# Kernel tuning notes

Hardware: AMD Instinct MI355X
Metric: run time of the kernel (lower is better)

Reference implementation:

```python
import jax, jax.numpy as jnp
import numpy as np

N, T, U, C, V = 8, 256, 64, 512, 1024

def setup_inputs() -> dict:
    key = jax.random.key(0)
    k1, k2, k3, k4 = jax.random.split(key, 4)
    encoder_out = jax.random.normal(k1, (N, T, C), dtype=jnp.float32)
    pred_out = jax.random.normal(k2, (N, U, C), dtype=jnp.float32)
    # nn.Linear(C, V): weight (V, C), bias (V,)
    bound = 1.0 / np.sqrt(C)
    W = jax.random.uniform(k3, (V, C), minval=-bound, maxval=bound, dtype=jnp.float32)
    b = jax.random.uniform(k4, (V,), minval=-bound, maxval=bound, dtype=jnp.float32)
    return {"encoder_out": encoder_out, "pred_out": pred_out, "W": W, "b": b}

def reference(encoder_out, pred_out, W, b):
    # broadcast add: (N,T,1,C) + (N,1,U,C) -> (N,T,U,C)
    x = jnp.tanh(encoder_out[:, :, None, :] + pred_out[:, None, :, :])
    # Linear projection to vocab: (N,T,U,C) @ (C,V) + b
    logits = jnp.einsum("ntuc,vc->ntuv", x, W) + b
    return logits
```

## Files before the change

### kernel.cpp

```cpp
#include <hip/hip_runtime.h>

#define C_DIM 512
#define V_DIM 1024

typedef __attribute__((ext_vector_type(8))) short short8;
typedef __attribute__((ext_vector_type(4))) float f32x4;

__device__ __forceinline__ short f2bf(float f) {
  unsigned int u = __float_as_uint(f);
  u += 0x7fffu + ((u >> 16) & 1u);
  return (short)(u >> 16);
}

__device__ __forceinline__ float fast_tanh_f(float x) {
  float e = __expf(2.0f * x);
  return fmaf(-2.0f, __builtin_amdgcn_rcpf(e + 1.0f), 1.0f);
}

__global__ __launch_bounds__(256) void wswz_kernel(const float* __restrict__ W,
                                                   char* __restrict__ wsw) {
  const int i = blockIdx.x * 256 + threadIdx.x;
  const int v = i >> 6;
  const int c0 = (i & 63) << 3;
  const float* wp = W + (size_t)v * C_DIM + c0;
  const f32x4 w0 = *(const f32x4*)(wp);
  const f32x4 w1 = *(const f32x4*)(wp + 4);
  short8 pk;
  pk[0] = f2bf(w0[0]); pk[1] = f2bf(w0[1]); pk[2] = f2bf(w0[2]); pk[3] = f2bf(w0[3]);
  pk[4] = f2bf(w1[0]); pk[5] = f2bf(w1[1]); pk[6] = f2bf(w1[2]); pk[7] = f2bf(w1[3]);
  const int vt = v >> 8, vloc = v & 255;
  const int kc = c0 >> 5, q = (c0 >> 3) & 3;
  char* dst = wsw + (size_t)(vt * 16 + kc) * 16384 + vloc * 64 + q * 16;
  *(short8*)dst = pk;
}

__global__ __launch_bounds__(256, 3) void joiner_kernel(
    const float* __restrict__ enc, const float* __restrict__ pred,
    const char* __restrict__ wsw, const float* __restrict__ bias,
    float* __restrict__ out) {
  __shared__ char abuf[2][4096];
  const int tid = threadIdx.x;
  const int lane = tid & 63;
  const int wn = tid >> 6;
  const int l15 = lane & 15, qd = lane >> 4;

  const int bid = blockIdx.x;
  const int wk = ((bid & 7) << 10) | (bid >> 3);
  const int rp = wk >> 2;
  const int vt = wk & 3;
  const int n = rp >> 8;

  const float* pe = enc + (size_t)rp * C_DIM + (tid & 3) * 8;
  const float* pp = pred + ((size_t)(n << 6) + (tid >> 2)) * C_DIM + (tid & 3) * 8;
  char* adst = &abuf[0][0] + tid * 16;

  const char* wbase = wsw + (size_t)vt * (16 * 16384) + (size_t)(wn * 64 + l15) * 64 + qd * 16;

  const char* afr = &abuf[0][0] + l15 * 64 + qd * 16;

  f32x4 acc[4][4];
#pragma unroll
  for (int mt = 0; mt < 4; ++mt)
#pragma unroll
    for (int nt = 0; nt < 4; ++nt) acc[mt][nt] = (f32x4){0.f, 0.f, 0.f, 0.f};

  short8 bfr[2][4];

  {
    const f32x4 e0 = *(const f32x4*)(pe);
    const f32x4 e1 = *(const f32x4*)(pe + 4);
    const f32x4 p0 = *(const f32x4*)(pp);
    const f32x4 p1 = *(const f32x4*)(pp + 4);
    short8 pk;
    pk[0] = f2bf(fast_tanh_f(e0[0] + p0[0]));
    pk[1] = f2bf(fast_tanh_f(e0[1] + p0[1]));
    pk[2] = f2bf(fast_tanh_f(e0[2] + p0[2]));
    pk[3] = f2bf(fast_tanh_f(e0[3] + p0[3]));
    pk[4] = f2bf(fast_tanh_f(e1[0] + p1[0]));
    pk[5] = f2bf(fast_tanh_f(e1[1] + p1[1]));
    pk[6] = f2bf(fast_tanh_f(e1[2] + p1[2]));
    pk[7] = f2bf(fast_tanh_f(e1[3] + p1[3]));
    *(short8*)(adst) = pk;
  }
#pragma unroll
  for (int nt = 0; nt < 4; ++nt)
    bfr[0][nt] = *(const short8*)(wbase + nt * 1024);
  __syncthreads();

#pragma unroll 2
  for (int kc = 0; kc < 16; ++kc) {
    const int cb = kc & 1, nb = cb ^ 1;

    f32x4 e0, e1, p0, p1;
    if (kc < 15) {
      const float* pe1 = pe + (kc + 1) * 32;
      const float* pp1 = pp + (kc + 1) * 32;
      e0 = *(const f32x4*)(pe1);
      e1 = *(const f32x4*)(pe1 + 4);
      p0 = *(const f32x4*)(pp1);
      p1 = *(const f32x4*)(pp1 + 4);
#pragma unroll
      for (int nt = 0; nt < 4; ++nt)
        bfr[nb][nt] = *(const short8*)(wbase + (kc + 1) * 16384 + nt * 1024);
    }

    const char* ab = afr + cb * 4096;
    const short8 a0 = *(const short8*)(ab);
    const short8 a1 = *(const short8*)(ab + 1024);
    const short8 a2 = *(const short8*)(ab + 2048);
    const short8 a3 = *(const short8*)(ab + 3072);

    acc[0][0] = __builtin_amdgcn_mfma_f32_16x16x32_bf16(a0, bfr[cb][0], acc[0][0], 0, 0, 0);
    acc[0][1] = __builtin_amdgcn_mfma_f32_16x16x32_bf16(a0, bfr[cb][1], acc[0][1], 0, 0, 0);
    acc[0][2] = __builtin_amdgcn_mfma_f32_16x16x32_bf16(a0, bfr[cb][2], acc[0][2], 0, 0, 0);
    acc[0][3] = __builtin_amdgcn_mfma_f32_16x16x32_bf16(a0, bfr[cb][3], acc[0][3], 0, 0, 0);
    acc[1][0] = __builtin_amdgcn_mfma_f32_16x16x32_bf16(a1, bfr[cb][0], acc[1][0], 0, 0, 0);
    acc[1][1] = __builtin_amdgcn_mfma_f32_16x16x32_bf16(a1, bfr[cb][1], acc[1][1], 0, 0, 0);
    acc[1][2] = __builtin_amdgcn_mfma_f32_16x16x32_bf16(a1, bfr[cb][2], acc[1][2], 0, 0, 0);
    acc[1][3] = __builtin_amdgcn_mfma_f32_16x16x32_bf16(a1, bfr[cb][3], acc[1][3], 0, 0, 0);
    acc[2][0] = __builtin_amdgcn_mfma_f32_16x16x32_bf16(a2, bfr[cb][0], acc[2][0], 0, 0, 0);
    acc[2][1] = __builtin_amdgcn_mfma_f32_16x16x32_bf16(a2, bfr[cb][1], acc[2][1], 0, 0, 0);
    acc[2][2] = __builtin_amdgcn_mfma_f32_16x16x32_bf16(a2, bfr[cb][2], acc[2][2], 0, 0, 0);
    acc[2][3] = __builtin_amdgcn_mfma_f32_16x16x32_bf16(a2, bfr[cb][3], acc[2][3], 0, 0, 0);
    acc[3][0] = __builtin_amdgcn_mfma_f32_16x16x32_bf16(a3, bfr[cb][0], acc[3][0], 0, 0, 0);
    acc[3][1] = __builtin_amdgcn_mfma_f32_16x16x32_bf16(a3, bfr[cb][1], acc[3][1], 0, 0, 0);
    acc[3][2] = __builtin_amdgcn_mfma_f32_16x16x32_bf16(a3, bfr[cb][2], acc[3][2], 0, 0, 0);
    acc[3][3] = __builtin_amdgcn_mfma_f32_16x16x32_bf16(a3, bfr[cb][3], acc[3][3], 0, 0, 0);

    if (kc < 15) {
      short8 pk;
      pk[0] = f2bf(fast_tanh_f(e0[0] + p0[0]));
      pk[1] = f2bf(fast_tanh_f(e0[1] + p0[1]));
      pk[2] = f2bf(fast_tanh_f(e0[2] + p0[2]));
      pk[3] = f2bf(fast_tanh_f(e0[3] + p0[3]));
      pk[4] = f2bf(fast_tanh_f(e1[0] + p1[0]));
      pk[5] = f2bf(fast_tanh_f(e1[1] + p1[1]));
      pk[6] = f2bf(fast_tanh_f(e1[2] + p1[2]));
      pk[7] = f2bf(fast_tanh_f(e1[3] + p1[3]));
      *(short8*)(adst + nb * 4096) = pk;
    }
    __syncthreads();
  }

  const int colb = (vt << 8) + (wn << 6) + l15;
  const size_t r0 = ((size_t)rp << 6) + (qd << 2);
#pragma unroll
  for (int nt = 0; nt < 4; ++nt) {
    const float bb = bias[colb + nt * 16];
#pragma unroll
    for (int mt = 0; mt < 4; ++mt) {
      float* op = out + (r0 + mt * 16) * V_DIM + colb + nt * 16;
      op[0 * V_DIM] = acc[mt][nt][0] + bb;
      op[1 * V_DIM] = acc[mt][nt][1] + bb;
      op[2 * V_DIM] = acc[mt][nt][2] + bb;
      op[3 * V_DIM] = acc[mt][nt][3] + bb;
    }
  }
}

extern "C" void kernel_launch(void* const* d_in, const int* in_sizes, int n_in,
                              void* d_out, int out_size, void* d_ws, size_t ws_size,
                              hipStream_t stream) {
  const float* enc  = (const float*)d_in[0];
  const float* pred = (const float*)d_in[1];
  const float* W    = (const float*)d_in[2];
  const float* bias = (const float*)d_in[3];
  float* out = (float*)d_out;
  char* wsw = (char*)d_ws;

  wswz_kernel<<<dim3(256), dim3(256), 0, stream>>>(W, wsw);
  joiner_kernel<<<dim3(8192), dim3(256), 0, stream>>>(enc, pred, wsw, bias, out);
}
```

Baseline: 699.6 us.

## Stage full tanh A-tile in LDS once and loop over all vocab tiles

Each block now computes the full 64x512 tanh activation for one (n,t) row into 64KB of dynamic LDS once, then loops over all four vocab tiles, instead of recomputing the activation per vocab tile across four separate blocks. The MFMA switches from 16x16x32 to 32x32x16 bf16, and the weight swizzle is changed to match the new fragment layout. It also adds s_setprio around the MFMA bursts and uses nontemporal output stores. The costs are lower occupancy (2 blocks per CU, large LDS) and a serial activation prologue that no longer overlaps with the MFMA work.

```diff
diff --git a/kernel.cpp b/kernel.cpp
--- a/kernel.cpp
+++ b/kernel.cpp
@@ -5,6 +5,7 @@
 
 typedef __attribute__((ext_vector_type(8))) short short8;
 typedef __attribute__((ext_vector_type(4))) float f32x4;
+typedef __attribute__((ext_vector_type(16))) float f32x16;
 
 __device__ __forceinline__ short f2bf(float f) {
   unsigned int u = __float_as_uint(f);
@@ -29,105 +30,41 @@
   pk[0] = f2bf(w0[0]); pk[1] = f2bf(w0[1]); pk[2] = f2bf(w0[2]); pk[3] = f2bf(w0[3]);
   pk[4] = f2bf(w1[0]); pk[5] = f2bf(w1[1]); pk[6] = f2bf(w1[2]); pk[7] = f2bf(w1[3]);
   const int vt = v >> 8, vloc = v & 255;
-  const int kc = c0 >> 5, q = (c0 >> 3) & 3;
-  char* dst = wsw + (size_t)(vt * 16 + kc) * 16384 + vloc * 64 + q * 16;
+  const int wn = vloc >> 6, nt = (vloc >> 5) & 1, c32 = vloc & 31;
+  const int kc = c0 >> 5, s = (c0 >> 4) & 1, hi = (c0 >> 3) & 1;
+  char* dst = wsw + (size_t)(vt * 16 + kc) * 16384 +
+              wn * 4096 + nt * 2048 + s * 1024 + hi * 512 + c32 * 16;
   *(short8*)dst = pk;
 }
 
-__global__ __launch_bounds__(256, 3) void joiner_kernel(
+__global__ __launch_bounds__(256, 2) void joiner_kernel(
     const float* __restrict__ enc, const float* __restrict__ pred,
     const char* __restrict__ wsw, const float* __restrict__ bias,
     float* __restrict__ out) {
-  __shared__ char abuf[2][4096];
+  extern __shared__ char smem[];
   const int tid = threadIdx.x;
   const int lane = tid & 63;
   const int wn = tid >> 6;
-  const int l15 = lane & 15, qd = lane >> 4;
+  const int l31 = lane & 31, hf = lane >> 5;
 
   const int bid = blockIdx.x;
-  const int wk = ((bid & 7) << 10) | (bid >> 3);
-  const int rp = wk >> 2;
-  const int vt = wk & 3;
+  const int rp = ((bid & 7) << 8) | (bid >> 3);
   const int n = rp >> 8;
 
-  const float* pe = enc + (size_t)rp * C_DIM + (tid & 3) * 8;
-  const float* pp = pred + ((size_t)(n << 6) + (tid >> 2)) * C_DIM + (tid & 3) * 8;
-  char* adst = &abuf[0][0] + tid * 16;
-
-  const char* wbase = wsw + (size_t)vt * (16 * 16384) + (size_t)(wn * 64 + l15) * 64 + qd * 16;
-
-  const char* afr = &abuf[0][0] + l15 * 64 + qd * 16;
-
-  f32x4 acc[4][4];
-#pragma unroll
-  for (int mt = 0; mt < 4; ++mt)
-#pragma unroll
-    for (int nt = 0; nt < 4; ++nt) acc[mt][nt] = (f32x4){0.f, 0.f, 0.f, 0.f};
-
-  short8 bfr[2][4];
-
   {
-    const f32x4 e0 = *(const f32x4*)(pe);
-    const f32x4 e1 = *(const f32x4*)(pe + 4);
-    const f32x4 p0 = *(const f32x4*)(pp);
-    const f32x4 p1 = *(const f32x4*)(pp + 4);
-    short8 pk;
-    pk[0] = f2bf(fast_tanh_f(e0[0] + p0[0]));
-    pk[1] = f2bf(fast_tanh_f(e0[1] + p0[1]));
-    pk[2] = f2bf(fast_tanh_f(e0[2] + p0[2]));
-    pk[3] = f2bf(fast_tanh_f(e0[3] + p0[3]));
-    pk[4] = f2bf(fast_tanh_f(e1[0] + p1[0]));
-    pk[5] = f2bf(fast_tanh_f(e1[1] + p1[1]));
-    pk[6] = f2bf(fast_tanh_f(e1[2] + p1[2]));
-    pk[7] = f2bf(fast_tanh_f(e1[3] + p1[3]));
-    *(short8*)(adst) = pk;
-  }
-#pragma unroll
-  for (int nt = 0; nt < 4; ++nt)
-    bfr[0][nt] = *(const short8*)(wbase + nt * 1024);
-  __syncthreads();
-
-#pragma unroll 2
-  for (int kc = 0; kc < 16; ++kc) {
-    const int cb = kc & 1, nb = cb ^ 1;
-
-    f32x4 e0, e1, p0, p1;
-    if (kc < 15) {
-      const float* pe1 = pe + (kc + 1) * 32;
-      const float* pp1 = pp + (kc + 1) * 32;
-      e0 = *(const f32x4*)(pe1);
-      e1 = *(const f32x4*)(pe1 + 4);
-      p0 = *(const f32x4*)(pp1);
-      p1 = *(const f32x4*)(pp1 + 4);
-#pragma unroll
-      for (int nt = 0; nt < 4; ++nt)
-        bfr[nb][nt] = *(const short8*)(wbase + (kc + 1) * 16384 + nt * 1024);
-    }
-
-    const char* ab = afr + cb * 4096;
-    const short8 a0 = *(const short8*)(ab);
-    const short8 a1 = *(const short8*)(ab + 1024);
-    const short8 a2 = *(const short8*)(ab + 2048);
-    const short8 a3 = *(const short8*)(ab + 3072);
-
-    acc[0][0] = __builtin_amdgcn_mfma_f32_16x16x32_bf16(a0, bfr[cb][0], acc[0][0], 0, 0, 0);
-    acc[0][1] = __builtin_amdgcn_mfma_f32_16x16x32_bf16(a0, bfr[cb][1], acc[0][1], 0, 0, 0);
-    acc[0][2] = __builtin_amdgcn_mfma_f32_16x16x32_bf16(a0, bfr[cb][2], acc[0][2], 0, 0, 0);
-    acc[0][3] = __builtin_amdgcn_mfma_f32_16x16x32_bf16(a0, bfr[cb][3], acc[0][3], 0, 0, 0);
-    acc[1][0] = __builtin_amdgcn_mfma_f32_16x16x32_bf16(a1, bfr[cb][0], acc[1][0], 0, 0, 0);
-    acc[1][1] = __builtin_amdgcn_mfma_f32_16x16x32_bf16(a1, bfr[cb][1], acc[1][1], 0, 0, 0);
-    acc[1][2] = __builtin_amdgcn_mfma_f32_16x16x32_bf16(a1, bfr[cb][2], acc[1][2], 0, 0, 0);
-    acc[1][3] = __builtin_amdgcn_mfma_f32_16x16x32_bf16(a1, bfr[cb][3], acc[1][3], 0, 0, 0);
-    acc[2][0] = __builtin_amdgcn_mfma_f32_16x16x32_bf16(a2, bfr[cb][0], acc[2][0], 0, 0, 0);
-    acc[2][1] = __builtin_amdgcn_mfma_f32_16x16x32_bf16(a2, bfr[cb][1], acc[2][1], 0, 0, 0);
-    acc[2][2] = __builtin_amdgcn_mfma_f32_16x16x32_bf16(a2, bfr[cb][2], acc[2][2], 0, 0, 0);
-    acc[2][3] = __builtin_amdgcn_mfma_f32_16x16x32_bf16(a2, bfr[cb][3], acc[2][3], 0, 0, 0);
-    acc[3][0] = __builtin_amdgcn_mfma_f32_16x16x32_bf16(a3, bfr[cb][0], acc[3][0], 0, 0, 0);
-    acc[3][1] = __builtin_amdgcn_mfma_f32_16x16x32_bf16(a3, bfr[cb][1], acc[3][1], 0, 0, 0);
-    acc[3][2] = __builtin_amdgcn_mfma_f32_16x16x32_bf16(a3, bfr[cb][2], acc[3][2], 0, 0, 0);
-    acc[3][3] = __builtin_amdgcn_mfma_f32_16x16x32_bf16(a3, bfr[cb][3], acc[3][3], 0, 0, 0);
-
-    if (kc < 15) {
+    const int mt_s = tid >> 7;
+    const int rr = tid & 31;
+    const int u = mt_s * 32 + rr;
+    const int koff = ((tid >> 6) & 1) * 16 + ((tid >> 5) & 1) * 8;
+    const float* pe = enc + (size_t)rp * C_DIM + koff;
+    const float* pp = pred + ((size_t)(n * 64 + u)) * C_DIM + koff;
+    char* adst = smem + tid * 16;
+#pragma unroll 4
+    for (int kc = 0; kc < 16; ++kc) {
+      const f32x4 e0 = *(const f32x4*)(pe + kc * 32);
+      const f32x4 e1 = *(const f32x4*)(pe + kc * 32 + 4);
+      const f32x4 p0 = *(const f32x4*)(pp + kc * 32);
+      const f32x4 p1 = *(const f32x4*)(pp + kc * 32 + 4);
       short8 pk;
       pk[0] = f2bf(fast_tanh_f(e0[0] + p0[0]));
       pk[1] = f2bf(fast_tanh_f(e0[1] + p0[1]));
@@ -137,23 +74,75 @@
       pk[5] = f2bf(fast_tanh_f(e1[1] + p1[1]));
       pk[6] = f2bf(fast_tanh_f(e1[2] + p1[2]));
       pk[7] = f2bf(fast_tanh_f(e1[3] + p1[3]));
-      *(short8*)(adst + nb * 4096) = pk;
+      *(short8*)(adst + kc * 4096) = pk;
     }
-    __syncthreads();
+  }
+  __syncthreads();
+
+  const char* ab = smem + hf * 512 + l31 * 16;
+  const char* wb = wsw + wn * 4096 + hf * 512 + l31 * 16;
+
+  f32x16 acc[2][2];
+#pragma unroll
+  for (int mt = 0; mt < 2; ++mt)
+#pragma unroll
+    for (int nt = 0; nt < 2; ++nt)
+#pragma unroll
+      for (int r = 0; r < 16; ++r) acc[mt][nt][r] = 0.0f;
+
+  short8 afr[2][4], bfr[2][4];
+
+#pragma unroll
+  for (int f = 0; f < 4; ++f) {
+    bfr[0][f] = *(const short8*)(wb + f * 1024);
+    afr[0][f] = *(const short8*)(ab + f * 1024);
   }
 
-  const int colb = (vt << 8) + (wn << 6) + l15;
-  const size_t r0 = ((size_t)rp << 6) + (qd << 2);
+  for (int vt = 0; vt < 4; ++vt) {
+    const char* wg = wb + (size_t)vt * 262144;
 #pragma unroll
-  for (int nt = 0; nt < 4; ++nt) {
-    const float bb = bias[colb + nt * 16];
+    for (int kc = 0; kc < 16; ++kc) {
+      const int cb = kc & 1, nb = cb ^ 1;
+
+      if (kc < 15 || vt < 3) {
+        const char* bp = wg + (kc + 1) * 16384;
+        const char* ap = ab + ((kc + 1) & 15) * 4096;
 #pragma unroll
-    for (int mt = 0; mt < 4; ++mt) {
-      float* op = out + (r0 + mt * 16) * V_DIM + colb + nt * 16;
-      op[0 * V_DIM] = acc[mt][nt][0] + bb;
-      op[1 * V_DIM] = acc[mt][nt][1] + bb;
-      op[2 * V_DIM] = acc[mt][nt][2] + bb;
-      op[3 * V_DIM] = acc[mt][nt][3] + bb;
+        for (int f = 0; f < 4; ++f) {
+          bfr[nb][f] = *(const short8*)(bp + f * 1024);
+          afr[nb][f] = *(const short8*)(ap + f * 1024);
+        }
+      }
+
+      __builtin_amdgcn_s_setprio(1);
+#pragma unroll
+      for (int s = 0; s < 2; ++s)
+#pragma unroll
+        for (int mt = 0; mt < 2; ++mt)
+#pragma unroll
+          for (int nt = 0; nt < 2; ++nt)
+            acc[mt][nt] = __builtin_amdgcn_mfma_f32_32x32x16_bf16(
+                afr[cb][mt * 2 + s], bfr[cb][nt * 2 + s], acc[mt][nt], 0, 0, 0);
+      __builtin_amdgcn_s_setprio(0);
+    }
+
+    {
+      const int colb = (vt << 8) + (wn << 6) + l31;
+      float* ob = out + ((size_t)rp * 64 + hf * 4) * V_DIM + colb;
+#pragma unroll
+      for (int nt = 0; nt < 2; ++nt) {
+        const float bb = bias[colb + nt * 32];
+#pragma unroll
+        for (int mt = 0; mt < 2; ++mt) {
+#pragma unroll
+          for (int r = 0; r < 16; ++r) {
+            const int row_off = mt * 32 + (r & 3) + 8 * (r >> 2);
+            __builtin_nontemporal_store(acc[mt][nt][r] + bb,
+                                        ob + (size_t)row_off * V_DIM + nt * 32);
+            acc[mt][nt][r] = 0.0f;
+          }
+        }
+      }
     }
   }
 }
@@ -169,5 +158,8 @@
   char* wsw = (char*)d_ws;
 
   wswz_kernel<<<dim3(256), dim3(256), 0, stream>>>(W, wsw);
-  joiner_kernel<<<dim3(8192), dim3(256), 0, stream>>>(enc, pred, wsw, bias, out);
+
+  (void)hipFuncSetAttribute((const void*)joiner_kernel,
+                            hipFuncAttributeMaxDynamicSharedMemorySize, 65536);
+  joiner_kernel<<<dim3(2048), dim3(256), 65536, stream>>>(enc, pred, wsw, bias, out);
 }
```

Measured after the change: 629.0 us. -10.1%, faster.
